# Kernel tuning notes

Hardware: AMD Instinct MI355X
Metric: run time of the kernel (lower is better)

Reference implementation:

```python
import jax, jax.numpy as jnp
import numpy as np

N_PATHS = 100000
N_STEPS = 512          # number of Euler steps; paths have N_STEPS+1 time points
DT = 0.004             # step_size (~1/250, daily)
KAPPA = 1.0
THETA = 0.04
SIGMA = 0.2
RHO = -0.7
S0 = 100.0
V0 = 0.04


def setup_inputs() -> dict:
    key = jax.random.key(0)
    z = jax.random.normal(key, (N_PATHS, N_STEPS, 2), dtype=jnp.float32)
    return {"z": z}


def reference(z):
    # Euler-Maruyama simulation of the Heston SDE with full-truncation clamp:
    #   dS = S * sqrt(v) dW1
    #   dv = kappa*(theta - v) dt + sigma*sqrt(v) dW2,  corr(dW1,dW2)=rho
    sqdt = jnp.sqrt(jnp.float32(DT))
    c = jnp.sqrt(jnp.float32(1.0 - RHO * RHO))

    def step(carry, zt):
        s, v = carry                      # each [N]
        vp = jnp.maximum(v, 0.0)
        sv = jnp.sqrt(vp)
        dW1 = sqdt * zt[:, 0]
        dW2 = RHO * dW1 + c * sqdt * zt[:, 1]
        s_new = s + s * sv * dW1
        v_new = jnp.maximum(v + KAPPA * (THETA - vp) * DT + SIGMA * sv * dW2, 0.0)
        return (s_new, v_new), (s_new, v_new)

    s0 = jnp.full((N_PATHS,), S0, dtype=z.dtype)
    v0 = jnp.full((N_PATHS,), V0, dtype=z.dtype)
    _, (ss, vs) = jax.lax.scan(step, (s0, v0), jnp.transpose(z, (1, 0, 2)))

    prices = jnp.concatenate([s0[None], ss], axis=0).T      # [N, T+1]
    variances = jnp.concatenate([v0[None], vs], axis=0).T   # [N, T+1]

    # variance-swap price: cumsum of variance * dt + analytic remaining leg L
    tau = jnp.linspace(N_STEPS * DT, 0.0, N_STEPS + 1).astype(z.dtype)  # [T+1]
    L = (variances - THETA) / KAPPA * (1.0 - jnp.exp(-KAPPA * tau)) + THETA * tau
    varswap = jnp.cumsum(variances, axis=1) * DT + L        # [N, T+1]

    # [N, T+1, 3] = (price, variance, varswap price)
    return jnp.stack([prices, variances, varswap], axis=-1)
```

## Files before the change

kernel.cpp:

```cpp
#include <hip/hip_runtime.h>


#define N_PATHS 100000
#define N_STEPS 512
#define TROW    1539
#define CSTEP   16
#define NCHUNK  (N_STEPS / CSTEP)
#define PB      64
#define ZSTR    34
#define OSTR    49

__global__ __launch_bounds__(PB, 2)
void heston_kernel(const float* __restrict__ z, float* __restrict__ out) {
    __shared__ float zl[PB * ZSTR];
    __shared__ float ol[PB * OSTR];

    const int tid = threadIdx.x;
    const int p0  = blockIdx.x * PB;
    const int lim = N_PATHS - p0;
    const bool ragged = (lim < PB);

    const float DTc   = 0.004f;
    const float THETA = 0.04f;
    const float SIGMA = 0.2f;
    const float RHO   = -0.7f;
    const float S0c   = 100.0f;
    const float V0c   = 0.04f;
    const float sqdt  = 0.06324555320f;
    const float csdt  = 0.71414284285f * 0.06324555320f;
    const float TAU0  = 2.048f;
    const float EDT   = expf(DTc);
    const float E0    = expf(-TAU0);

    int voff[8];
    #pragma unroll
    for (int j = 0; j < 8; ++j) {
        int pj = p0 + (tid >> 3) + 8 * j;
        if (pj > N_PATHS - 1) pj = N_PATHS - 1;
        voff[j] = pj * 4096 + (tid & 7) * 16;
    }
    const char* zb = (const char*)z;

    {
        float4 f[8];
        #pragma unroll
        for (int j = 0; j < 8; ++j) f[j] = *(const float4*)(zb + voff[j]);
        #pragma unroll
        for (int j = 0; j < 8; ++j) {
            float2* d = (float2*)&zl[((tid >> 3) + 8 * j) * ZSTR + (tid & 7) * 4];
            d[0] = make_float2(f[j].x, f[j].y);
            d[1] = make_float2(f[j].z, f[j].w);
        }
    }

    {
        const float vs0 = fmaf(V0c, DTc, fmaf(THETA, TAU0, (V0c - THETA) * (1.0f - E0)));
        #pragma unroll
        for (int k = 0; k < 3; ++k) {
            int idx = k * PB + tid;
            int pl = idx / 3, si = idx - pl * 3;
            if (pl < lim)
                out[(p0 + pl) * TROW + si] = (si == 0) ? S0c : (si == 1) ? V0c : vs0;
        }
    }

    int gof[3], lof[3];
    {
        int pl = (tid >= 48) ? 1 : 0;
        int si = tid - pl * 48;
        #pragma unroll
        for (int j = 0; j < 3; ++j) {
            gof[j] = pl * TROW + si;
            lof[j] = pl * OSTR + si;
            pl += 1; si += 16;
            if (si >= 48) { si -= 48; pl += 1; }
        }
    }

    float s   = S0c;
    float v   = V0c;
    float acc = V0c;
    float tau = TAU0;
    float e   = E0;

    __syncthreads();

    for (int c = 0; c < NCHUNK; ++c) {
        const int cn = ((c < NCHUNK - 1) ? (c + 1) : (NCHUNK - 1)) * 128;
        float4 f[8];
        #pragma unroll
        for (int j = 0; j < 8; ++j) f[j] = *(const float4*)(zb + voff[j] + cn);

        #pragma unroll
        for (int dt = 0; dt < CSTEP; ++dt) {
            const float2 zz = *(const float2*)&zl[tid * ZSTR + 2 * dt];
            const float vp  = fmaxf(v, 0.0f);
            const float sv  = __builtin_amdgcn_sqrtf(vp);
            const float dW1 = sqdt * zz.x;
            const float dW2 = fmaf(RHO, dW1, csdt * zz.y);
            s = fmaf(s * sv, dW1, s);
            v = fmaxf(fmaf(SIGMA * sv, dW2, fmaf(THETA - vp, DTc, v)), 0.0f);
            acc += v;
            tau -= DTc;
            e *= EDT;
            const float vs = fmaf(acc, DTc, fmaf(THETA, tau, (v - THETA) * (1.0f - e)));
            ol[tid * OSTR + 3 * dt    ] = s;
            ol[tid * OSTR + 3 * dt + 1] = v;
            ol[tid * OSTR + 3 * dt + 2] = vs;
        }

        __syncthreads();

        if (!ragged) {
            float* oc = out + (size_t)p0 * TROW + 3 + 48 * c;
            #pragma unroll
            for (int g = 0; g < 16; ++g) {
                #pragma unroll
                for (int j = 0; j < 3; ++j) {
                    oc[gof[j] + g * (4 * TROW)] = ol[lof[j] + g * (4 * OSTR)];
                }
            }
        } else {
            for (int k = 0; k < 48; ++k) {
                int idx = k * PB + tid;
                int pl2 = idx / 48, si2 = idx - pl2 * 48;
                if (pl2 < lim)
                    out[(size_t)(p0 + pl2) * TROW + 3 + 48 * c + si2] = ol[pl2 * OSTR + si2];
            }
        }

        #pragma unroll
        for (int j = 0; j < 8; ++j) {
            float2* d = (float2*)&zl[((tid >> 3) + 8 * j) * ZSTR + (tid & 7) * 4];
            d[0] = make_float2(f[j].x, f[j].y);
            d[1] = make_float2(f[j].z, f[j].w);
        }
        __syncthreads();
    }
}

extern "C" void kernel_launch(void* const* d_in, const int* in_sizes, int n_in,
                              void* d_out, int out_size, void* d_ws, size_t ws_size,
                              hipStream_t stream) {
    const float* z = (const float*)d_in[0];
    float* out = (float*)d_out;
    const int nblocks = (N_PATHS + PB - 1) / PB;
    heston_kernel<<<nblocks, PB, 0, stream>>>(z, out);
}
```

Measured before the change: 385.6 us.

## Deepen z prefetch to two chunks and drop block barriers for single-wave blocks

The kernel now keeps two register buffers of upcoming z chunks, so the global loads for chunk c+2 are in flight while chunk c is computed and written out. Both `__syncthreads` calls go away, relying on the 64-thread block being a single wavefront so shared-memory reads and writes stay ordered. The `launch_bounds` min-blocks hint is also removed. The goal is to hide global load latency and cut barrier stalls in this memory-bound kernel. The cost is more register pressure, and correctness depends on no LDS reordering within the wave and on the compiler not moving shared accesses without a fence.

```diff
diff --git a/kernel.cpp b/kernel.cpp
--- a/kernel.cpp
+++ b/kernel.cpp
@@ -10,7 +10,9 @@
 #define ZSTR    34
 #define OSTR    49
 
-__global__ __launch_bounds__(PB, 2)
+typedef float f32x4 __attribute__((ext_vector_type(4)));
+
+__global__ __launch_bounds__(PB)
 void heston_kernel(const float* __restrict__ z, float* __restrict__ out) {
     __shared__ float zl[PB * ZSTR];
     __shared__ float ol[PB * OSTR];
@@ -41,17 +43,11 @@
     }
     const char* zb = (const char*)z;
 
-    {
-        float4 f[8];
-        #pragma unroll
-        for (int j = 0; j < 8; ++j) f[j] = *(const float4*)(zb + voff[j]);
-        #pragma unroll
-        for (int j = 0; j < 8; ++j) {
-            float2* d = (float2*)&zl[((tid >> 3) + 8 * j) * ZSTR + (tid & 7) * 4];
-            d[0] = make_float2(f[j].x, f[j].y);
-            d[1] = make_float2(f[j].z, f[j].w);
-        }
-    }
+    f32x4 fA[8], fB[8];
+    #pragma unroll
+    for (int j = 0; j < 8; ++j) fA[j] = *(const f32x4*)(zb + voff[j]);
+    #pragma unroll
+    for (int j = 0; j < 8; ++j) fB[j] = *(const f32x4*)(zb + voff[j] + 128);
 
     {
         const float vs0 = fmaf(V0c, DTc, fmaf(THETA, TAU0, (V0c - THETA) * (1.0f - E0)));
@@ -60,7 +56,7 @@
             int idx = k * PB + tid;
             int pl = idx / 3, si = idx - pl * 3;
             if (pl < lim)
-                out[(p0 + pl) * TROW + si] = (si == 0) ? S0c : (si == 1) ? V0c : vs0;
+                out[(size_t)(p0 + pl) * TROW + si] = (si == 0) ? S0c : (si == 1) ? V0c : vs0;
         }
     }
 
@@ -77,19 +73,21 @@
         }
     }
 
-    float s   = S0c;
-    float v   = V0c;
-    float acc = V0c;
-    float tau = TAU0;
-    float e   = E0;
+    #pragma unroll
+    for (int j = 0; j < 8; ++j) {
+        float2* d = (float2*)&zl[((tid >> 3) + 8 * j) * ZSTR + (tid & 7) * 4];
+        d[0] = make_float2(fA[j].x, fA[j].y);
+        d[1] = make_float2(fA[j].z, fA[j].w);
+    }
 
-    __syncthreads();
+    float s = S0c, v = V0c, acc = V0c, tau = TAU0, e = E0;
 
-    for (int c = 0; c < NCHUNK; ++c) {
-        const int cn = ((c < NCHUNK - 1) ? (c + 1) : (NCHUNK - 1)) * 128;
-        float4 f[8];
-        #pragma unroll
-        for (int j = 0; j < 8; ++j) f[j] = *(const float4*)(zb + voff[j] + cn);
+    auto chunk = [&](int c, f32x4 (&fn)[8], f32x4 (&fw)[8]) {
+        if (c + 2 < NCHUNK) {
+            const int cn = (c + 2) * 128;
+            #pragma unroll
+            for (int j = 0; j < 8; ++j) fn[j] = *(const f32x4*)(zb + voff[j] + cn);
+        }
 
         #pragma unroll
         for (int dt = 0; dt < CSTEP; ++dt) {
@@ -108,8 +106,6 @@
             ol[tid * OSTR + 3 * dt + 1] = v;
             ol[tid * OSTR + 3 * dt + 2] = vs;
         }
-
-        __syncthreads();
 
         if (!ragged) {
             float* oc = out + (size_t)p0 * TROW + 3 + 48 * c;
@@ -132,10 +128,14 @@
         #pragma unroll
         for (int j = 0; j < 8; ++j) {
             float2* d = (float2*)&zl[((tid >> 3) + 8 * j) * ZSTR + (tid & 7) * 4];
-            d[0] = make_float2(f[j].x, f[j].y);
-            d[1] = make_float2(f[j].z, f[j].w);
+            d[0] = make_float2(fw[j].x, fw[j].y);
+            d[1] = make_float2(fw[j].z, fw[j].w);
         }
-        __syncthreads();
+    };
+
+    for (int cc = 0; cc < NCHUNK; cc += 2) {
+        chunk(cc,     fA, fB);
+        chunk(cc + 1, fB, fA);
     }
 }
 
```

New measurement: 385.6 us. About the same (+0.0%).
